# Performance work log

Hardware: AMD Instinct MI355X
Metric: run time of the kernel (lower is better)

Reference implementation:

```python
import jax, jax.numpy as jnp
import numpy as np


def setup_inputs() -> dict:
    key = jax.random.key(0)
    k1, k2 = jax.random.split(key)
    B, D = 8192, 256
    pred = jax.random.normal(k1, (B, D), dtype=jnp.float32)
    gt = jax.random.normal(k2, (B, D), dtype=jnp.float32)
    sigma = jnp.ones((), dtype=jnp.float32)  # learned scalar param (dim=1, mode='auto')
    return {"pred": pred, "gt": gt, "sigma": sigma}


def reference(pred, gt, sigma):
    # p, g: [B, D] (flatten from start_dim=1 is identity for 2D inputs)
    p = pred.reshape(pred.shape[0], -1)
    g = gt.reshape(gt.shape[0], -1)
    B, D = p.shape
    noise_var = sigma ** 2
    # MVN(mean=p_i, cov=noise_var*I).log_prob(g_j) in closed form:
    # -0.5 * ||g_j - p_i||^2 / noise_var - 0.5 * D * log(2*pi*noise_var)
    sq_dist = (
        jnp.sum(p * p, axis=-1)[:, None]
        + jnp.sum(g * g, axis=-1)[None, :]
        - 2.0 * (p @ g.T)
    )  # [B, B]
    log_norm = 0.5 * D * jnp.log(2.0 * jnp.pi * noise_var)
    logits = -0.5 * sq_dist / noise_var - log_norm  # [B, B], class dim = 1
    # cross_entropy(logits, arange(B)) = mean_i(-log_softmax(logits)[i, i])
    logp = jax.nn.log_softmax(logits, axis=1)
    loss = -jnp.mean(jnp.diagonal(logp))
    loss = loss * jax.lax.stop_gradient(2.0 * noise_var)
    return loss
```

## Files before the change

### kernel.cpp

```cpp
#include <hip/hip_runtime.h>
#include <hip/hip_fp8.h>


typedef float f32x4 __attribute__((ext_vector_type(4)));
typedef float f32x16 __attribute__((ext_vector_type(16)));
typedef int i32x4 __attribute__((ext_vector_type(4)));
typedef int i32x8 __attribute__((ext_vector_type(8)));

#define LN2F 0.6931471805599453f
#define LOG2EF 1.4426950408889634f
#define NB 8192
#define ND 256
#define NCHUNK 32

#define AS1 __attribute__((address_space(1)))
#define AS3 __attribute__((address_space(3)))

__device__ __forceinline__ float fexp2(float x) {
#if __has_builtin(__builtin_amdgcn_exp2f)
  return __builtin_amdgcn_exp2f(x);
#else
  float r;
  asm("v_exp_f32 %0, %1\n\ts_nop 1" : "=v"(r) : "v"(x));
  return r;
#endif
}

__device__ __forceinline__ int pack4_fp8(float a, float b, float c, float d) {
#if __has_builtin(__builtin_amdgcn_cvt_pk_fp8_f32)
  int w = __builtin_amdgcn_cvt_pk_fp8_f32(a, b, 0, false);
  w = __builtin_amdgcn_cvt_pk_fp8_f32(c, d, w, true);
  return w;
#else
  unsigned b0 = __hip_fp8_e4m3(a).__x, b1 = __hip_fp8_e4m3(b).__x;
  unsigned b2 = __hip_fp8_e4m3(c).__x, b3 = __hip_fp8_e4m3(d).__x;
  return (int)(b0 | (b1 << 8) | (b2 << 16) | (b3 << 24));
#endif
}

__global__ __launch_bounds__(256) void vmse_prep(
    const float* __restrict__ pred, const float* __restrict__ gt,
    const float* __restrict__ sigma,
    unsigned char* __restrict__ Ah, unsigned char* __restrict__ Bh,
    float* __restrict__ diag, float* __restrict__ gnorm,
    float* __restrict__ ghs)
{
  const float nv = sigma[0] * sigma[0];
  const float s = LOG2EF / nv;
  const int row = blockIdx.x * 4 + (threadIdx.x >> 6);
  const int l = threadIdx.x & 63;
  const float4 p = *(const float4*)(pred + row * ND + l * 4);
  const float4 g = *(const float4*)(gt   + row * ND + l * 4);
  const int pw = pack4_fp8(p.x * s, p.y * s, p.z * s, p.w * s);
  const int gw = pack4_fp8(g.x, g.y, g.z, g.w);
  *(int*)(Ah + row * ND + l * 4) = pw;
  *(int*)(Bh + row * ND + l * 4) = gw;
  float dd = p.x * g.x + p.y * g.y + p.z * g.z + p.w * g.w;
  float gg = g.x * g.x + g.y * g.y + g.z * g.z + g.w * g.w;
  #pragma unroll
  for (int off = 1; off < 64; off <<= 1) {
    dd += __shfl_xor(dd, off);
    gg += __shfl_xor(gg, off);
  }
  if (l == 0) {
    diag[row] = dd;
    gnorm[row] = gg;
    ghs[row] = -0.5f * s * gg;
  }
}

__device__ __forceinline__ void epi16(const f32x16& acc, float& m, float& l) {
  const float mx0 = fmaxf(fmaxf(acc[0], acc[1]), fmaxf(acc[2], acc[3]));
  const float mx1 = fmaxf(fmaxf(acc[4], acc[5]), fmaxf(acc[6], acc[7]));
  const float mx2 = fmaxf(fmaxf(acc[8], acc[9]), fmaxf(acc[10], acc[11]));
  const float mx3 = fmaxf(fmaxf(acc[12], acc[13]), fmaxf(acc[14], acc[15]));
  const float tmax = fmaxf(fmaxf(mx0, mx1), fmaxf(mx2, mx3));
  if (__any(tmax > m + 8.0f)) {
    const float nm = fmaxf(m, tmax);
    l *= fexp2(m - nm);
    m = nm;
  }
  const float e0 = (fexp2(acc[0] - m) + fexp2(acc[1] - m)) +
                   (fexp2(acc[2] - m) + fexp2(acc[3] - m));
  const float e1 = (fexp2(acc[4] - m) + fexp2(acc[5] - m)) +
                   (fexp2(acc[6] - m) + fexp2(acc[7] - m));
  const float e2 = (fexp2(acc[8] - m) + fexp2(acc[9] - m)) +
                   (fexp2(acc[10] - m) + fexp2(acc[11] - m));
  const float e3 = (fexp2(acc[12] - m) + fexp2(acc[13] - m)) +
                   (fexp2(acc[14] - m) + fexp2(acc[15] - m));
  l += (e0 + e1) + (e2 + e3);
}

__global__ __launch_bounds__(512, 4) void vmse_main(
    const unsigned char* __restrict__ Ah, const unsigned char* __restrict__ Bh,
    const float* __restrict__ ghs, float* __restrict__ partial)
{
  __shared__ unsigned char lds[8][32 * 256];
  __shared__ float lds_ghs[256];
  const int tid = threadIdx.x;
  const int lane = tid & 63;
  const int wid = tid >> 6;
  const int rb = blockIdx.x & 31;
  const int ch = blockIdx.x >> 5;
  const int r31 = lane & 31;
  const int hi = lane >> 5;
  const int j0 = ch * 256;

  {
    const int r = wid * 4 + (lane >> 4);
    const int cg = (lane & 15) ^ (r & 15);
    const unsigned char* src = Bh + (size_t)(j0 + r) * ND + cg * 16;
    #pragma unroll
    for (int t = 0; t < 8; ++t)
      __builtin_amdgcn_global_load_lds(
          (const AS1 unsigned int*)(src + t * 8192),
          (AS3 unsigned int*)&lds[t][wid * 1024], 16, 0, 0);
  }
  if (tid < 256) lds_ghs[tid] = ghs[j0 + tid];

  i32x8 pf[4];
  {
    const unsigned char* prow = Ah + (size_t)((rb * 256) + (wid * 32) + r31) * ND;
    #pragma unroll
    for (int m = 0; m < 4; ++m)
      pf[m] = *(const i32x8*)(prow + m * 64 + hi * 32);
  }

  const int sl = r31 & 3;
  const int sh = (r31 >> 2) & 3;
  const char* ldsc = (const char*)&lds[0][0];
  const char* pj0 = ldsc + r31 * 256 + (((hi * 2) ^ sl) * 16);
  const char* pj1 = ldsc + r31 * 256 + (((hi * 2 + 1) ^ sl) * 16);
  const char* pg0[4];
  const char* pg1[4];
  #pragma unroll
  for (int m = 0; m < 4; ++m) {
    pg0[m] = pj0 + ((m ^ sh) << 6);
    pg1[m] = pj1 + ((m ^ sh) << 6);
  }

  float m2 = -3.0e38f, l2 = 0.0f;

  __syncthreads();

  const char* gbase = (const char*)lds_ghs + hi * 16;

  #define TILE(ACC, tile)                                                    \
    {                                                                        \
      _Pragma("unroll")                                                      \
      for (int q = 0; q < 4; ++q) {                                          \
        const f32x4 gv = *(const f32x4*)(gbase + (tile) * 128 + q * 32);     \
        ACC[4 * q + 0] = gv[0];                                              \
        ACC[4 * q + 1] = gv[1];                                              \
        ACC[4 * q + 2] = gv[2];                                              \
        ACC[4 * q + 3] = gv[3];                                              \
      }                                                                      \
      _Pragma("unroll")                                                      \
      for (int m = 0; m < 4; ++m) {                                          \
        const i32x4 a0 = *(const i32x4*)(pg0[m] + (tile) * 8192);            \
        const i32x4 a1 = *(const i32x4*)(pg1[m] + (tile) * 8192);            \
        const i32x8 ga = {a0[0], a0[1], a0[2], a0[3],                        \
                          a1[0], a1[1], a1[2], a1[3]};                       \
        ACC = __builtin_amdgcn_mfma_scale_f32_32x32x64_f8f6f4(               \
            ga, pf[m], ACC, 0, 0, 0, 0x7F7F7F7F, 0, 0x7F7F7F7F);             \
      }                                                                      \
    }

  f32x16 accA, accB;
  TILE(accA, 0);
  #pragma unroll
  for (int i = 0; i < 4; ++i) {
    TILE(accB, 2 * i + 1);
    epi16(accA, m2, l2);
    if (2 * i + 2 < 8) {
      TILE(accA, 2 * i + 2);
    }
    epi16(accB, m2, l2);
  }

  {
    const float om = __shfl_xor(m2, 32);
    const float ol = __shfl_xor(l2, 32);
    const float nm = fmaxf(m2, om);
    l2 = l2 * fexp2(m2 - nm) + ol * fexp2(om - nm);
    m2 = nm;
    if (hi == 0) {
      const int row = rb * 256 + wid * 32 + r31;
      partial[row * NCHUNK + ch] = m2 + log2f(l2);
    }
  }
}

__global__ __launch_bounds__(256) void vmse_combine(
    const float* __restrict__ partial, const float* __restrict__ diag,
    const float* __restrict__ gnorm, const float* __restrict__ sigma,
    float* __restrict__ bsum)
{
  const int r = blockIdx.x * 256 + threadIdx.x;
  const float nv = sigma[0] * sigma[0];
  float p[NCHUNK];
  float M = -3.0e38f;
  #pragma unroll
  for (int c = 0; c < NCHUNK; ++c) { p[c] = partial[r * NCHUNK + c]; M = fmaxf(M, p[c]); }
  float ssum = 0.f;
  #pragma unroll
  for (int c = 0; c < NCHUNK; ++c) ssum += exp2f(p[c] - M);
  const float lse2 = M + log2f(ssum);
  const float zii = (diag[r] - 0.5f * gnorm[r]) / nv;
  float contrib = LN2F * lse2 - zii;
  #pragma unroll
  for (int off = 1; off < 64; off <<= 1) contrib += __shfl_xor(contrib, off);
  __shared__ float wsum[4];
  if ((threadIdx.x & 63) == 0) wsum[threadIdx.x >> 6] = contrib;
  __syncthreads();
  if (threadIdx.x == 0)
    bsum[blockIdx.x] = (wsum[0] + wsum[1]) + (wsum[2] + wsum[3]);
}

__global__ __launch_bounds__(64) void vmse_final(
    const float* __restrict__ bsum, const float* __restrict__ sigma,
    float* __restrict__ out)
{
  const int lane = threadIdx.x;
  float v = (lane < 32) ? bsum[lane] : 0.f;
  #pragma unroll
  for (int off = 1; off < 64; off <<= 1) v += __shfl_xor(v, off);
  if (lane == 0) {
    const float nv = sigma[0] * sigma[0];
    out[0] = v * (2.0f * nv / (float)NB);
  }
}

extern "C" void kernel_launch(void* const* d_in, const int* in_sizes, int n_in,
                              void* d_out, int out_size, void* d_ws, size_t ws_size,
                              hipStream_t stream)
{
  const float* pred  = (const float*)d_in[0];
  const float* gt    = (const float*)d_in[1];
  const float* sigma = (const float*)d_in[2];
  char* ws = (char*)d_ws;
  unsigned char* Ah = (unsigned char*)(ws);
  unsigned char* Bh = (unsigned char*)(ws + (2u << 20));
  float* gnorm   = (float*)(ws + (4u << 20));
  float* diag    = (float*)(ws + (4u << 20) + (32u << 10));
  float* ghs     = (float*)(ws + (4u << 20) + (64u << 10));
  float* partial = (float*)(ws + (4u << 20) + (96u << 10));
  float* bsum    = (float*)(ws + (4u << 20) + (96u << 10) + (1u << 20));

  vmse_prep<<<NB / 4, 256, 0, stream>>>(pred, gt, sigma, Ah, Bh, diag, gnorm, ghs);
  vmse_main<<<32 * NCHUNK, 512, 0, stream>>>(Ah, Bh, ghs, partial);
  vmse_combine<<<NB / 256, 256, 0, stream>>>(partial, diag, gnorm, sigma, bsum);
  vmse_final<<<1, 64, 0, stream>>>(bsum, sigma, (float*)d_out);
}
```

Before: 38.47 us.

## Process two 32-row A tiles per wave to reuse each LDS B fragment

Each wave now holds two sets of pred fp8 fragments (64 rows instead of 32), so every B fragment read from LDS feeds two MFMAs. The grid is halved to 512 blocks, and each block covers 512 rows against a 256-column chunk. The goal is to halve LDS reads and global B staging per unit of MFMA work. In exchange it doubles accumulator and fragment register use, which may reduce occupancy under launch_bounds(512,4). It also drops the previous software pipelining that overlapped the epilogue with the next tile.

```diff
diff --git a/kernel.cpp b/kernel.cpp
--- a/kernel.cpp
+++ b/kernel.cpp
@@ -100,8 +100,8 @@
   const int tid = threadIdx.x;
   const int lane = tid & 63;
   const int wid = tid >> 6;
-  const int rb = blockIdx.x & 31;
-  const int ch = blockIdx.x >> 5;
+  const int rb = blockIdx.x & 15;
+  const int ch = blockIdx.x >> 4;
   const int r31 = lane & 31;
   const int hi = lane >> 5;
   const int j0 = ch * 256;
@@ -118,12 +118,16 @@
   }
   if (tid < 256) lds_ghs[tid] = ghs[j0 + tid];
 
-  i32x8 pf[4];
-  {
-    const unsigned char* prow = Ah + (size_t)((rb * 256) + (wid * 32) + r31) * ND;
-    #pragma unroll
-    for (int m = 0; m < 4; ++m)
-      pf[m] = *(const i32x8*)(prow + m * 64 + hi * 32);
+  i32x8 pfA[4], pfB[4];
+  {
+    const unsigned char* prowA =
+        Ah + (size_t)((rb * 512) + (wid * 64) + r31) * ND;
+    const unsigned char* prowB = prowA + 32 * ND;
+    #pragma unroll
+    for (int m = 0; m < 4; ++m) {
+      pfA[m] = *(const i32x8*)(prowA + m * 64 + hi * 32);
+      pfB[m] = *(const i32x8*)(prowB + m * 64 + hi * 32);
+    }
   }
 
   const int sl = r31 & 3;
@@ -139,54 +143,56 @@
     pg1[m] = pj1 + ((m ^ sh) << 6);
   }
 
-  float m2 = -3.0e38f, l2 = 0.0f;
+  float mA = -3.0e38f, lA = 0.0f;
+  float mB = -3.0e38f, lB = 0.0f;
 
   __syncthreads();
 
   const char* gbase = (const char*)lds_ghs + hi * 16;
 
-  #define TILE(ACC, tile)                                                    \
-    {                                                                        \
-      _Pragma("unroll")                                                      \
-      for (int q = 0; q < 4; ++q) {                                          \
-        const f32x4 gv = *(const f32x4*)(gbase + (tile) * 128 + q * 32);     \
-        ACC[4 * q + 0] = gv[0];                                              \
-        ACC[4 * q + 1] = gv[1];                                              \
-        ACC[4 * q + 2] = gv[2];                                              \
-        ACC[4 * q + 3] = gv[3];                                              \
-      }                                                                      \
-      _Pragma("unroll")                                                      \
-      for (int m = 0; m < 4; ++m) {                                          \
-        const i32x4 a0 = *(const i32x4*)(pg0[m] + (tile) * 8192);            \
-        const i32x4 a1 = *(const i32x4*)(pg1[m] + (tile) * 8192);            \
-        const i32x8 ga = {a0[0], a0[1], a0[2], a0[3],                        \
-                          a1[0], a1[1], a1[2], a1[3]};                       \
-        ACC = __builtin_amdgcn_mfma_scale_f32_32x32x64_f8f6f4(               \
-            ga, pf[m], ACC, 0, 0, 0, 0x7F7F7F7F, 0, 0x7F7F7F7F);             \
-      }                                                                      \
-    }
-
-  f32x16 accA, accB;
-  TILE(accA, 0);
-  #pragma unroll
-  for (int i = 0; i < 4; ++i) {
-    TILE(accB, 2 * i + 1);
-    epi16(accA, m2, l2);
-    if (2 * i + 2 < 8) {
-      TILE(accA, 2 * i + 2);
-    }
-    epi16(accB, m2, l2);
-  }
-
-  {
-    const float om = __shfl_xor(m2, 32);
-    const float ol = __shfl_xor(l2, 32);
-    const float nm = fmaxf(m2, om);
-    l2 = l2 * fexp2(m2 - nm) + ol * fexp2(om - nm);
-    m2 = nm;
+  #pragma unroll
+  for (int tile = 0; tile < 8; ++tile) {
+    f32x16 accA, accB;
+    #pragma unroll
+    for (int q = 0; q < 4; ++q) {
+      const f32x4 gv = *(const f32x4*)(gbase + tile * 128 + q * 32);
+      accA[4 * q + 0] = gv[0]; accA[4 * q + 1] = gv[1];
+      accA[4 * q + 2] = gv[2]; accA[4 * q + 3] = gv[3];
+    }
+    accB = accA;
+    #pragma unroll
+    for (int m = 0; m < 4; ++m) {
+      const i32x4 a0 = *(const i32x4*)(pg0[m] + tile * 8192);
+      const i32x4 a1 = *(const i32x4*)(pg1[m] + tile * 8192);
+      const i32x8 ga = {a0[0], a0[1], a0[2], a0[3],
+                        a1[0], a1[1], a1[2], a1[3]};
+      accA = __builtin_amdgcn_mfma_scale_f32_32x32x64_f8f6f4(
+          ga, pfA[m], accA, 0, 0, 0, 0x7F7F7F7F, 0, 0x7F7F7F7F);
+      accB = __builtin_amdgcn_mfma_scale_f32_32x32x64_f8f6f4(
+          ga, pfB[m], accB, 0, 0, 0, 0x7F7F7F7F, 0, 0x7F7F7F7F);
+    }
+    epi16(accA, mA, lA);
+    epi16(accB, mB, lB);
+  }
+
+  {
+    const float om = __shfl_xor(mA, 32);
+    const float ol = __shfl_xor(lA, 32);
+    const float nm = fmaxf(mA, om);
+    lA = lA * fexp2(mA - nm) + ol * fexp2(om - nm);
     if (hi == 0) {
-      const int row = rb * 256 + wid * 32 + r31;
-      partial[row * NCHUNK + ch] = m2 + log2f(l2);
+      const int row = rb * 512 + wid * 64 + r31;
+      partial[row * NCHUNK + ch] = nm + log2f(lA);
+    }
+  }
+  {
+    const float om = __shfl_xor(mB, 32);
+    const float ol = __shfl_xor(lB, 32);
+    const float nm = fmaxf(mB, om);
+    lB = lB * fexp2(mB - nm) + ol * fexp2(om - nm);
+    if (hi == 0) {
+      const int row = rb * 512 + wid * 64 + 32 + r31;
+      partial[row * NCHUNK + ch] = nm + log2f(lB);
     }
   }
 }
@@ -248,7 +254,7 @@
   float* bsum    = (float*)(ws + (4u << 20) + (96u << 10) + (1u << 20));
 
   vmse_prep<<<NB / 4, 256, 0, stream>>>(pred, gt, sigma, Ah, Bh, diag, gnorm, ghs);
-  vmse_main<<<32 * NCHUNK, 512, 0, stream>>>(Ah, Bh, ghs, partial);
+  vmse_main<<<16 * NCHUNK, 512, 0, stream>>>(Ah, Bh, ghs, partial);
   vmse_combine<<<NB / 256, 256, 0, stream>>>(partial, diag, gnorm, sigma, bsum);
   vmse_final<<<1, 64, 0, stream>>>(bsum, sigma, (float*)d_out);
 }
```

Measured after the change: 74.62 us. 93.9% more time.

## Prefetch LDS operand tiles into registers one tile ahead of MFMA

Applied to the files above, without the earlier changes.

The main loop now loads the next tile's LDS fragments into double-buffered registers before running the MFMAs and softmax epilogue on the current tile. The goal is to hide LDS load latency behind compute. The occupancy hint in launch bounds drops from 4 to 2 waves per SIMD so the extra prefetch registers fit, which may reduce latency hiding from concurrent waves.

```diff
diff --git a/kernel.cpp b/kernel.cpp
--- a/kernel.cpp
+++ b/kernel.cpp
@@ -91,7 +91,7 @@
   l += (e0 + e1) + (e2 + e3);
 }
 
-__global__ __launch_bounds__(512, 4) void vmse_main(
+__global__ __launch_bounds__(512, 2) void vmse_main(
     const unsigned char* __restrict__ Ah, const unsigned char* __restrict__ Bh,
     const float* __restrict__ ghs, float* __restrict__ partial)
 {
@@ -145,7 +145,16 @@
 
   const char* gbase = (const char*)lds_ghs + hi * 16;
 
-  #define TILE(ACC, tile)                                                    \
+  #define LOADG(B0, B1, tile)                                                \
+    {                                                                        \
+      _Pragma("unroll")                                                      \
+      for (int m = 0; m < 4; ++m) {                                          \
+        B0[m] = *(const i32x4*)(pg0[m] + (tile) * 8192);                     \
+        B1[m] = *(const i32x4*)(pg1[m] + (tile) * 8192);                     \
+      }                                                                      \
+    }
+
+  #define TILEC(ACC, B0, B1, tile)                                           \
     {                                                                        \
       _Pragma("unroll")                                                      \
       for (int q = 0; q < 4; ++q) {                                          \
@@ -157,25 +166,29 @@
       }                                                                      \
       _Pragma("unroll")                                                      \
       for (int m = 0; m < 4; ++m) {                                          \
-        const i32x4 a0 = *(const i32x4*)(pg0[m] + (tile) * 8192);            \
-        const i32x4 a1 = *(const i32x4*)(pg1[m] + (tile) * 8192);            \
-        const i32x8 ga = {a0[0], a0[1], a0[2], a0[3],                        \
-                          a1[0], a1[1], a1[2], a1[3]};                       \
+        const i32x8 ga = {B0[m][0], B0[m][1], B0[m][2], B0[m][3],            \
+                          B1[m][0], B1[m][1], B1[m][2], B1[m][3]};           \
         ACC = __builtin_amdgcn_mfma_scale_f32_32x32x64_f8f6f4(               \
             ga, pf[m], ACC, 0, 0, 0, 0x7F7F7F7F, 0, 0x7F7F7F7F);             \
       }                                                                      \
     }
 
-  f32x16 accA, accB;
-  TILE(accA, 0);
+  i32x4 gA0[4], gA1[4], gB0[4], gB1[4];
+  LOADG(gA0, gA1, 0);
   #pragma unroll
   for (int i = 0; i < 4; ++i) {
-    TILE(accB, 2 * i + 1);
-    epi16(accA, m2, l2);
-    if (2 * i + 2 < 8) {
-      TILE(accA, 2 * i + 2);
-    }
-    epi16(accB, m2, l2);
+    LOADG(gB0, gB1, 2 * i + 1);
+    {
+      f32x16 acc;
+      TILEC(acc, gA0, gA1, 2 * i);
+      epi16(acc, m2, l2);
+    }
+    if (2 * i + 2 < 8) LOADG(gA0, gA1, 2 * i + 2);
+    {
+      f32x16 acc;
+      TILEC(acc, gB0, gB1, 2 * i + 1);
+      epi16(acc, m2, l2);
+    }
   }
 
   {
```

Result: no change. 38.39 us (-0.2%).
